# Kernel optimization log

Measured on AMD Instinct MI355X. Metric: run time of the kernel, lower is better.

Reference implementation:

```python
import jax, jax.numpy as jnp
import numpy as np

B, T, V, E, H, C = 128, 256, 50000, 300, 512, 11
START, STOP = 9, 10
NEG = -100000.0


def _lstm_dir(x, mask, w_ih, w_hh, b_ih, b_hh, reverse):
    # x: [B,T,D]; precompute input-to-gate projection for all timesteps
    gx = jnp.einsum('btd,gd->btg', x, w_ih) + b_ih + b_hh
    m = mask
    if reverse:
        gx = gx[:, ::-1]
        m = m[:, ::-1]
    Bc = x.shape[0]
    Hh = w_hh.shape[1]

    def step(carry, inp):
        h, c = carry
        g, mt = inp
        gates = g + h @ w_hh.T  # [B,4H]
        i, f, gg, o = jnp.split(gates, 4, axis=-1)
        i = jax.nn.sigmoid(i)
        f = jax.nn.sigmoid(f)
        o = jax.nn.sigmoid(o)
        gg = jnp.tanh(gg)
        c_new = f * c + i * gg
        h_new = o * jnp.tanh(c_new)
        mt = mt[:, None]
        h = jnp.where(mt, h_new, h)  # packed-sequence semantics: hold state on pads
        c = jnp.where(mt, c_new, c)
        return (h, c), h

    init = (jnp.zeros((Bc, Hh), x.dtype), jnp.zeros((Bc, Hh), x.dtype))
    _, hs = jax.lax.scan(step, init, (gx.transpose(1, 0, 2), m.T))
    hs = hs.transpose(1, 0, 2)
    if reverse:
        hs = hs[:, ::-1]
    # pad_packed_sequence zeroes padded positions
    return hs * mask[..., None].astype(x.dtype)


def _encode(tokens, mask, embeddings, params):
    x = embeddings[tokens]
    for (wif, whf, bif, bhf, wir, whr, bir, bhr) in params:
        fwd = _lstm_dir(x, mask, wif, whf, bif, bhf, False)
        bwd = _lstm_dir(x, mask, wir, whr, bir, bhr, True)
        x = jnp.concatenate([fwd, bwd], -1)
    return x


def _viterbi(emis, mask, transitions, seq_len):
    def vstep(scores, inp):
        emi, mt = inp
        cand = scores[:, :, None] + transitions[None]  # [B,C,C]
        bt = jnp.argmax(cand, axis=1)
        new = jnp.max(cand, axis=1) + emi
        return jnp.where(mt[:, None], new, scores), bt

    scores0 = jnp.zeros_like(emis[:, 0, :])
    final, backtrack = jax.lax.scan(vstep, scores0, (emis.transpose(1, 0, 2), mask.T))
    final = final + transitions[:, STOP][None]
    best_last = jnp.argmax(final, axis=-1)  # [B]

    ls = jnp.arange(emis.shape[1] - 1, -1, -1)

    def btstep(cur, inp):
        bt_l, l = inp
        emit = jnp.where(l < seq_len, cur, 0)  # pad tail with 0 as in original
        prev = jnp.take_along_axis(bt_l, cur[:, None], axis=1)[:, 0]
        cur = jnp.where((l >= 1) & (l <= seq_len - 1), prev, cur)
        return cur, emit

    _, emits = jax.lax.scan(btstep, best_last, (backtrack[::-1], ls))
    return emits[::-1].T  # [B,T]


def _nll(emis, tags, mask, transitions, seq_len):
    # CRF forward algorithm (replicates original init with -1e5 full scores)
    def fstep(scores, inp):
        emi, mt = inp
        new = jax.nn.logsumexp(scores[:, :, None] + emi[:, None, :] + transitions[None], axis=1)
        return jnp.where(mt[:, None], new, scores), None

    scores0 = jnp.full_like(emis[:, 0, :], NEG)
    final, _ = jax.lax.scan(fstep, scores0, (emis.transpose(1, 0, 2), mask.T))
    fwd_score = jax.nn.logsumexp(final + transitions[:, STOP][None], axis=-1, keepdims=True)

    em_sc = jnp.take_along_axis(emis, tags[..., None], -1)[..., 0]  # [B,T]
    y_aug = jnp.concatenate([jnp.full((tags.shape[0], 1), START, tags.dtype), tags], 1)
    tr_sc = transitions[y_aug[:, :-1], y_aug[:, 1:]]  # [B,T]
    last_tag = jnp.take_along_axis(y_aug, seq_len[:, None], 1)
    last_tr = transitions[last_tag[:, 0], STOP][:, None]
    mf = mask.astype(emis.dtype)
    gold = (mf * (em_sc + tr_sc)).sum(-1, keepdims=True) + last_tr
    return (fwd_score - gold).mean()


def setup_inputs() -> dict:
    key = jax.random.key(0)
    ks = iter(jax.random.split(key, 40))
    sl = jax.random.randint(next(ks), (B,), 1, T + 1)
    sl = -jnp.sort(-sl.at[0].set(T))  # descending, max == T (pack_padded requirement)
    mask = jnp.arange(T)[None, :] < sl[:, None]
    tokens = jax.random.randint(next(ks), (B, T), 0, V)
    tags = jax.random.randint(next(ks), (B, T), 0, 9)
    s = 1.0 / float(np.sqrt(H))

    def u(shape):
        return jax.random.uniform(next(ks), shape, jnp.float32, -s, s)

    inp = dict(tokens=tokens, seq_len=sl, mask=mask, tags=tags,
               embeddings=jax.random.normal(next(ks), (V, E), jnp.float32) * 0.1)
    G = 4 * H
    for li, d in enumerate([E, 2 * H]):
        for suf in ['', 'r']:
            inp[f'w_ih_l{li}{suf}'] = u((G, d))
            inp[f'w_hh_l{li}{suf}'] = u((G, H))
            inp[f'b_ih_l{li}{suf}'] = u((G,))
            inp[f'b_hh_l{li}{suf}'] = u((G,))
    inp['fc_w'] = u((C, 2 * H))
    inp['fc_b'] = u((C,))
    tr = jax.random.normal(next(ks), (C, C), jnp.float32)
    inp['transitions'] = tr.at[START, :].set(-1.0).at[:, STOP].set(-1.0)
    return inp


def reference(tokens, seq_len, mask, tags, embeddings,
              w_ih_l0, w_hh_l0, b_ih_l0, b_hh_l0,
              w_ih_l0r, w_hh_l0r, b_ih_l0r, b_hh_l0r,
              w_ih_l1, w_hh_l1, b_ih_l1, b_hh_l1,
              w_ih_l1r, w_hh_l1r, b_ih_l1r, b_hh_l1r,
              fc_w, fc_b, transitions):
    params = [(w_ih_l0, w_hh_l0, b_ih_l0, b_hh_l0, w_ih_l0r, w_hh_l0r, b_ih_l0r, b_hh_l0r),
              (w_ih_l1, w_hh_l1, b_ih_l1, b_hh_l1, w_ih_l1r, w_hh_l1r, b_ih_l1r, b_hh_l1r)]
    out = _encode(tokens, mask, embeddings, params)  # [B,T,2H]
    emis = jnp.einsum('bth,ch->btc', out, fc_w) + fc_b  # CRF fc (dropout=eval no-op)
    pred = _viterbi(emis, mask, transitions, seq_len)
    loss = _nll(emis, tags, mask, transitions, seq_len)
    return pred, loss
```

## Files before the change

kernel.cpp:

```cpp
#include <hip/hip_runtime.h>
#include <hip/hip_bf16.h>
#include <hip/hip_fp16.h>

#define BB   128
#define TT   256
#define EE   300
#define KP0  320
#define HH   512
#define GG   2048
#define NC   11
#define MM   (BB*TT)
#define START_TAG 9
#define STOP_TAG  10
#define NEGV (-100000.0f)

typedef _Float16 h2_t __attribute__((ext_vector_type(2)));
typedef _Float16 h4_t __attribute__((ext_vector_type(4)));
typedef _Float16 h8_t __attribute__((ext_vector_type(8)));
typedef float    f4_t __attribute__((ext_vector_type(4)));

__device__ __forceinline__ float sigf(float x) { return 1.0f / (1.0f + __expf(-x)); }

__global__ __launch_bounds__(256) void init_kernel(float* out, int* flags) {
    int t = threadIdx.x;
    if (t == 0) out[MM] = 0.0f;
    for (int i = t; i < 1024; i += 256) flags[i] = 0;
}

__global__ __launch_bounds__(256) void conv_pad_kernel(const float* __restrict__ W,
                                                       _Float16* __restrict__ O,
                                                       int K, int Kp4, int total4) {
    int idx = blockIdx.x * 256 + threadIdx.x;
    if (idx >= total4) return;
    int r = idx / Kp4, c4 = idx % Kp4, c = c4 * 4;
    h4_t v;
    if (c < K) {
        float4 f = *(const float4*)(W + (size_t)r * K + c);
        v[0] = (_Float16)f.x; v[1] = (_Float16)f.y; v[2] = (_Float16)f.z; v[3] = (_Float16)f.w;
    } else {
        v[0] = v[1] = v[2] = v[3] = (_Float16)0.0f;
    }
    *(h4_t*)(O + (size_t)r * (Kp4 * 4) + c) = v;
}

__global__ __launch_bounds__(256) void embed16_kernel(const int* __restrict__ tok,
                                                      const float* __restrict__ emb,
                                                      _Float16* __restrict__ x0,
                                                      int total4) {
    int idx = blockIdx.x * 256 + threadIdx.x;
    if (idx >= total4) return;
    int m = idx / (KP0 / 4), c4 = idx % (KP0 / 4), c = c4 * 4;
    h4_t v;
    if (c < EE) {
        float4 f = *(const float4*)(emb + (size_t)tok[m] * EE + c);
        v[0] = (_Float16)f.x; v[1] = (_Float16)f.y; v[2] = (_Float16)f.z; v[3] = (_Float16)f.w;
    } else {
        v[0] = v[1] = v[2] = v[3] = (_Float16)0.0f;
    }
    *(h4_t*)(x0 + (size_t)m * KP0 + c) = v;
}

#define LDA 72
__global__ __launch_bounds__(256) void gemm_bt_kernel(const _Float16* __restrict__ A,
                                                      const _Float16* __restrict__ Wf,
                                                      const float* __restrict__ b1,
                                                      const float* __restrict__ b2,
                                                      _Float16* __restrict__ C,
                                                      int Kp) {
    __shared__ __align__(16) char smem[36864];
    _Float16* As = (_Float16*)smem;
    _Float16* Bs = (_Float16*)(smem + 18432);
    const int tid = threadIdx.x;
    const int m0 = blockIdx.y * 128, n0 = blockIdx.x * 128;
    const int wv = tid >> 6, lane = tid & 63;
    const int wm = wv & 1, wn = wv >> 1;
    const int col = lane & 15, quad = lane >> 4;

    f4_t acc[4][4];
#pragma unroll
    for (int i = 0; i < 4; ++i)
#pragma unroll
        for (int j = 0; j < 4; ++j) acc[i][j] = (f4_t){0.f, 0.f, 0.f, 0.f};

    for (int k0 = 0; k0 < Kp; k0 += 64) {
#pragma unroll
        for (int cch = 0; cch < 4; ++cch) {
            int id = cch * 256 + tid;
            int row = id >> 3, cc = id & 7;
            h8_t va = *(const h8_t*)(A + (size_t)(m0 + row) * Kp + k0 + cc * 8);
            h8_t vb = *(const h8_t*)(Wf + (size_t)(n0 + row) * Kp + k0 + cc * 8);
            *(h8_t*)(As + row * LDA + cc * 8) = va;
            *(h8_t*)(Bs + row * LDA + cc * 8) = vb;
        }
        __syncthreads();
#pragma unroll
        for (int kk = 0; kk < 2; ++kk) {
            h8_t af[4], bf[4];
#pragma unroll
            for (int i = 0; i < 4; ++i) {
                af[i] = *(const h8_t*)(As + (wm * 64 + i * 16 + col) * LDA + kk * 32 + quad * 8);
                bf[i] = *(const h8_t*)(Bs + (wn * 64 + i * 16 + col) * LDA + kk * 32 + quad * 8);
            }
#pragma unroll
            for (int mi = 0; mi < 4; ++mi)
#pragma unroll
                for (int ni = 0; ni < 4; ++ni)
                    acc[mi][ni] = __builtin_amdgcn_mfma_f32_16x16x32_f16(af[mi], bf[ni], acc[mi][ni], 0, 0, 0);
        }
        __syncthreads();
    }

    _Float16* Ct = (_Float16*)smem;
#pragma unroll
    for (int ni = 0; ni < 4; ++ni) {
        int n = n0 + wn * 64 + ni * 16 + col;
        float bias = b1[n] + b2[n];
#pragma unroll
        for (int mi = 0; mi < 4; ++mi) {
#pragma unroll
            for (int r = 0; r < 4; ++r) {
                int mrow = wm * 64 + mi * 16 + quad * 4 + r;
                Ct[mrow * 136 + wn * 64 + ni * 16 + col] = (_Float16)(acc[mi][ni][r] + bias);
            }
        }
    }
    __syncthreads();
    {
        int row = tid >> 1, half = tid & 1;
#pragma unroll
        for (int cc2 = 0; cc2 < 8; ++cc2) {
            h8_t v = *(const h8_t*)(Ct + row * 136 + half * 64 + cc2 * 8);
            *(h8_t*)(C + (size_t)(m0 + row) * GG + n0 + half * 64 + cc2 * 8) = v;
        }
    }
}

__global__ __launch_bounds__(256, 1) void lstm_rec3_kernel(
        const _Float16* __restrict__ gx_f, const _Float16* __restrict__ gx_r,
        const float* __restrict__ whh_f, const float* __restrict__ whh_r,
        const int* __restrict__ seqlen, int c0, int nbg,
        _Float16* __restrict__ hs, _Float16* __restrict__ hbuf, int* __restrict__ flags) {
    extern __shared__ _Float16 Wlds[];
    _Float16* hstage = Wlds + 32768;

    const int wg = blockIdx.x;
    const int gs = wg & 15;
    const int grp = wg >> 4;
    const int bg = grp % nbg;
    const int dir = grp / nbg;
    const _Float16* gx = dir ? gx_r : gx_f;
    const float* W = dir ? whh_r : whh_f;
    int* myFlags = flags + grp * 16;
    _Float16* hb = hbuf + (size_t)grp * 2 * 16384;

    const int tid = threadIdx.x;
    const int wv = tid >> 6, lane = tid & 63;
    const int mt = wv & 1;
    const int p  = wv >> 1;
    const int col = lane & 15, quad = lane >> 4;

    for (int e = tid; e < 4096; e += 256) {
        int ln = e & 63, kc = (e >> 6) & 15, nt = e >> 10;
        int pp = nt >> 1;
        int n_in_pair = ((nt & 1) << 4) + (ln & 15);
        int gt = n_in_pair >> 3, jj = n_in_pair & 7;
        int R = gt * 512 + gs * 16 + pp * 8 + jj;
        int k = kc * 32 + (ln >> 4) * 8;
        const float4* src = (const float4*)(W + (size_t)R * 512 + k);
        float4 f0 = src[0], f1 = src[1];
        h8_t v;
        v[0] = (_Float16)f0.x; v[1] = (_Float16)f0.y; v[2] = (_Float16)f0.z; v[3] = (_Float16)f0.w;
        v[4] = (_Float16)f1.x; v[5] = (_Float16)f1.y; v[6] = (_Float16)f1.z; v[7] = (_Float16)f1.w;
        *(h8_t*)(Wlds + (size_t)e * 8) = v;
    }
    __syncthreads();

    const int maxsl = seqlen[c0 + bg * 32];
    int sl_r[4];
#pragma unroll
    for (int r = 0; r < 4; ++r) sl_r[r] = seqlen[c0 + bg * 32 + mt * 16 + quad * 4 + r];

    const int jglob = gs * 16 + p * 8 + (col & 7);
    const int hi = col >> 3;

    _Float16 pg0[4], pg1[4];
#pragma unroll
    for (int r = 0; r < 4; ++r) {
        pg0[r] = (_Float16)0.0f; pg1[r] = (_Float16)0.0f;
        if (0 < sl_r[r]) {
            int tm = dir ? (sl_r[r] - 1) : 0;
            int b_loc = bg * 32 + mt * 16 + quad * 4 + r;
            size_t base = ((size_t)(b_loc * TT + tm)) * GG;
            pg0[r] = gx[base + hi * 512 + jglob];
            pg1[r] = gx[base + 1024 + hi * 512 + jglob];
        }
    }

    if (tid < 128) {
        int m = tid >> 2, q = tid & 3;
        unsigned long long z = 0ull;
        const _Float16* dst = hb + 16384 + m * 512 + gs * 16 + q * 4;
        asm volatile("global_store_dwordx2 %0, %1, off sc0 sc1" :: "v"(dst), "v"(z) : "memory");
    }
    asm volatile("s_waitcnt vmcnt(0)" ::: "memory");
    __syncthreads();
    if (tid == 0) {
        int one = 1;
        asm volatile("global_store_dword %0, %1, off sc0 sc1" :: "v"(myFlags + gs), "v"(one) : "memory");
    }

    float cst[4] = {0.f, 0.f, 0.f, 0.f};
    float hst[4] = {0.f, 0.f, 0.f, 0.f};

    for (int s = 0; s < maxsl; ++s) {
        if (tid < 16) {
            const int* fp = myFlags + tid;
            int v, it = 0;
            for (;;) {
                asm volatile("global_load_dword %0, %1, off sc0 sc1\n\ts_waitcnt vmcnt(0)"
                             : "=v"(v) : "v"(fp) : "memory");
                if (v >= s + 1) break;
                if (it < 3) __builtin_amdgcn_s_sleep(1);
                else        __builtin_amdgcn_s_sleep(4);
                ++it;
            }
        }
        __syncthreads();

        const _Float16* hrd = hb + ((s + 1) & 1) * 16384;
        _Float16* hwr = hb + (s & 1) * 16384;

        h8_t a[16];
        const _Float16* ap = hrd + (mt * 16 + col) * 512 + quad * 8;
#pragma unroll
        for (int kc = 0; kc < 16; ++kc)
            asm volatile("global_load_dwordx4 %0, %1, off sc0 sc1"
                         : "=v"(a[kc]) : "v"(ap + kc * 32));
        asm volatile("s_waitcnt vmcnt(0)" ::: "memory");

        f4_t acc0 = {0.f, 0.f, 0.f, 0.f};
        f4_t acc1 = {0.f, 0.f, 0.f, 0.f};
#pragma unroll
        for (int kc = 0; kc < 16; ++kc) {
            h8_t b0 = *(const h8_t*)(Wlds + (((p * 2 + 0) * 16 + kc) * 64 + lane) * 8);
            h8_t b1 = *(const h8_t*)(Wlds + (((p * 2 + 1) * 16 + kc) * 64 + lane) * 8);
            acc0 = __builtin_amdgcn_mfma_f32_16x16x32_f16(a[kc], b0, acc0, 0, 0, 0);
            acc1 = __builtin_amdgcn_mfma_f32_16x16x32_f16(a[kc], b1, acc1, 0, 0, 0);
        }

#pragma unroll
        for (int r = 0; r < 4; ++r) {
            const bool valid = (s < sl_r[r]);
            float a0 = acc0[r] + (float)pg0[r];
            float a1 = acc1[r] + (float)pg1[r];
            float x0v = __shfl_xor(a0, 8);
            float x1v = __shfl_xor(a1, 8);
            float gi = hi ? x0v : a0;
            float gf = hi ? a0 : x0v;
            float gg2 = hi ? x1v : a1;
            float go = hi ? a1 : x1v;
            if (valid) {
                float cn = sigf(gf) * cst[r] + sigf(gi) * tanhf(gg2);
                cst[r] = cn;
                hst[r] = sigf(go) * tanhf(cn);
            }
            if (!hi)
                hstage[(mt * 16 + quad * 4 + r) * 16 + p * 8 + (col & 7)] = (_Float16)hst[r];
        }
        __syncthreads();

        if (tid < 128) {
            int m = tid >> 2, q = tid & 3;
            unsigned long long v = *(const unsigned long long*)(hstage + m * 16 + q * 4);
            const _Float16* dst = hwr + m * 512 + gs * 16 + q * 4;
            asm volatile("global_store_dwordx2 %0, %1, off sc0 sc1" :: "v"(dst), "v"(v) : "memory");
        }
        asm volatile("s_waitcnt vmcnt(0)" ::: "memory");
        __syncthreads();
        if (tid == 0) {
            int fv = s + 2;
            asm volatile("global_store_dword %0, %1, off sc0 sc1" :: "v"(myFlags + gs), "v"(fv) : "memory");
        }

#pragma unroll
        for (int r = 0; r < 4; ++r) {
            const bool valid = (s < sl_r[r]);
            if (valid && !hi) {
                int b_loc = bg * 32 + mt * 16 + quad * 4 + r;
                int tm = dir ? (sl_r[r] - 1 - s) : s;
                hs[((size_t)(b_loc * TT + tm) << 10) + (dir << 9) + jglob] = (_Float16)hst[r];
            }
        }
        {
            int sn = s + 1;
#pragma unroll
            for (int r = 0; r < 4; ++r) {
                pg0[r] = (_Float16)0.0f; pg1[r] = (_Float16)0.0f;
                if (sn < sl_r[r]) {
                    int tm = dir ? (sl_r[r] - 1 - sn) : sn;
                    int b_loc = bg * 32 + mt * 16 + quad * 4 + r;
                    size_t base = ((size_t)(b_loc * TT + tm)) * GG;
                    pg0[r] = gx[base + hi * 512 + jglob];
                    pg1[r] = gx[base + 1024 + hi * 512 + jglob];
                }
            }
        }
    }
}

__global__ __launch_bounds__(256) void emis_kernel(const _Float16* __restrict__ hs,
                                                   const float* __restrict__ fc_w,
                                                   const float* __restrict__ fc_b,
                                                   float* __restrict__ emis, int n) {
    int idx = blockIdx.x * 256 + threadIdx.x;
    if (idx >= n) return;
    int m = idx / NC, cc = idx % NC;
    const h8_t* a = (const h8_t*)(hs + (size_t)m * 1024);
    const float4* w = (const float4*)(fc_w + (size_t)cc * 1024);
    float s = 0.f;
#pragma unroll 4
    for (int k = 0; k < 128; ++k) {
        h8_t x = a[k];
        float4 y0 = w[2 * k], y1 = w[2 * k + 1];
        s += (float)x[0] * y0.x + (float)x[1] * y0.y + (float)x[2] * y0.z + (float)x[3] * y0.w;
        s += (float)x[4] * y1.x + (float)x[5] * y1.y + (float)x[6] * y1.z + (float)x[7] * y1.w;
    }
    emis[idx] = s + fc_b[cc];
}

__global__ __launch_bounds__(64) void crf_kernel(const float* __restrict__ emis,
                                                 const int* __restrict__ seq_len,
                                                 const int* __restrict__ tags,
                                                 const float* __restrict__ trans,
                                                 unsigned char* __restrict__ bt,
                                                 float* __restrict__ out, int c0) {
    const int b_loc = blockIdx.x;
    const int b = c0 + b_loc;
    const int lane = threadIdx.x;
    __shared__ float tr[NC * NC];
    for (int i = lane; i < NC * NC; i += 64) tr[i] = trans[i];
    __syncthreads();
    const int sl = seq_len[b];
    const bool act = lane < NC;
    const int jj = act ? lane : 0;

    float vs = 0.0f;
    float ns = NEGV;

    for (int t = 0; t < sl; ++t) {
        float ej = act ? emis[(size_t)(b_loc * TT + t) * NC + lane] : 0.0f;
        float vmax = -1e30f, nmax = -1e30f;
        int varg = 0;
        float nsave[NC];
#pragma unroll
        for (int i = 0; i < NC; ++i) {
            float vi = __shfl(vs, i);
            float ni = __shfl(ns, i);
            float tij = tr[i * NC + jj];
            float cv = vi + tij;
            if (cv > vmax) { vmax = cv; varg = i; }
            float cn = ni + tij;
            nsave[i] = cn;
            if (cn > nmax) nmax = cn;
        }
        float ssum = 0.f;
#pragma unroll
        for (int i = 0; i < NC; ++i) ssum += expf(nsave[i] - nmax);
        if (act) {
            vs = vmax + ej;
            ns = nmax + logf(ssum) + ej;
            bt[(size_t)(b_loc * TT + t) * NC + lane] = (unsigned char)varg;
        }
    }

    float finv = act ? vs + tr[lane * NC + STOP_TAG] : -1e30f;
    float finn = act ? ns + tr[lane * NC + STOP_TAG] : -1e30f;
    float vbest = -1e30f, fmax = -1e30f;
    int barg = 0;
#pragma unroll
    for (int j = 0; j < NC; ++j) {
        float v = __shfl(finv, j);
        if (v > vbest) { vbest = v; barg = j; }
        float n = __shfl(finn, j);
        if (n > fmax) fmax = n;
    }
    float fsum = 0.f;
#pragma unroll
    for (int j = 0; j < NC; ++j) fsum += expf(__shfl(finn, j) - fmax);
    float fwd = fmax + logf(fsum);

    float gsum = 0.f;
    for (int t = lane; t < sl; t += 64) {
        int tg = tags[b * TT + t];
        int pv = (t == 0) ? START_TAG : tags[b * TT + t - 1];
        gsum += emis[(size_t)(b_loc * TT + t) * NC + tg] + tr[pv * NC + tg];
    }
#pragma unroll
    for (int off = 32; off > 0; off >>= 1) gsum += __shfl_down(gsum, off);

    if (lane == 0) {
        float gold = gsum + tr[tags[b * TT + sl - 1] * NC + STOP_TAG];
        atomicAdd(out + MM, (fwd - gold) * (1.0f / (float)BB));
        int cur = barg;
        for (int l = sl - 1; l >= 0; --l) {
            out[b * TT + l] = (float)cur;
            if (l >= 1) cur = (int)bt[(size_t)(b_loc * TT + l) * NC + cur];
        }
    }
    for (int l = sl + lane; l < TT; l += 64) out[b * TT + l] = 0.0f;
}

extern "C" void kernel_launch(void* const* d_in, const int* in_sizes, int n_in,
                              void* d_out, int out_size, void* d_ws, size_t ws_size,
                              hipStream_t stream) {
    (void)in_sizes; (void)n_in; (void)out_size;
    const int* tokens = (const int*)d_in[0];
    const int* seqlen = (const int*)d_in[1];
    const int* tags = (const int*)d_in[3];
    const float* emb = (const float*)d_in[4];
    const float* w_ih_l0  = (const float*)d_in[5];
    const float* w_hh_l0  = (const float*)d_in[6];
    const float* b_ih_l0  = (const float*)d_in[7];
    const float* b_hh_l0  = (const float*)d_in[8];
    const float* w_ih_l0r = (const float*)d_in[9];
    const float* w_hh_l0r = (const float*)d_in[10];
    const float* b_ih_l0r = (const float*)d_in[11];
    const float* b_hh_l0r = (const float*)d_in[12];
    const float* w_ih_l1  = (const float*)d_in[13];
    const float* w_hh_l1  = (const float*)d_in[14];
    const float* b_ih_l1  = (const float*)d_in[15];
    const float* b_hh_l1  = (const float*)d_in[16];
    const float* w_ih_l1r = (const float*)d_in[17];
    const float* w_hh_l1r = (const float*)d_in[18];
    const float* b_ih_l1r = (const float*)d_in[19];
    const float* b_hh_l1r = (const float*)d_in[20];
    const float* fc_w  = (const float*)d_in[21];
    const float* fc_b  = (const float*)d_in[22];
    const float* trans = (const float*)d_in[23];

    const size_t per_b = 2097152u + 524288u + 163840u + 11264u + 2816u;
    const size_t fixed = 524288u + 4096u + 2u * 1310720u + 2u * 4194304u;
    int Bc = 128;
    while (Bc > 32 && fixed + per_b * (size_t)Bc > ws_size) Bc >>= 1;

    char* ws = (char*)d_ws;
    _Float16* hbuf = (_Float16*)ws;
    int* flags = (int*)(ws + 524288u);
    _Float16* w0f = (_Float16*)(ws + 528384u);
    _Float16* w0r = (_Float16*)(ws + 528384u + 1310720u);
    _Float16* w1f = (_Float16*)(ws + 528384u + 2u * 1310720u);
    _Float16* w1r = (_Float16*)(ws + 528384u + 2u * 1310720u + 4194304u);
    char* p = ws + fixed;
    _Float16* gxf   = (_Float16*)p;   p += (size_t)Bc * 1048576u;
    _Float16* gxr   = (_Float16*)p;   p += (size_t)Bc * 1048576u;
    _Float16* hs    = (_Float16*)p;   p += (size_t)Bc * 524288u;
    _Float16* x0f16 = (_Float16*)p;   p += (size_t)Bc * 163840u;
    float* emis     = (float*)p;      p += (size_t)Bc * 11264u;
    unsigned char* bt = (unsigned char*)p;
    float* out = (float*)d_out;

    init_kernel<<<1, 256, 0, stream>>>(out, flags);
    conv_pad_kernel<<<(2048 * 80 + 255) / 256, 256, 0, stream>>>(w_ih_l0,  w0f, EE, 80, 2048 * 80);
    conv_pad_kernel<<<(2048 * 80 + 255) / 256, 256, 0, stream>>>(w_ih_l0r, w0r, EE, 80, 2048 * 80);
    conv_pad_kernel<<<(2048 * 256 + 255) / 256, 256, 0, stream>>>(w_ih_l1,  w1f, 1024, 256, 2048 * 256);
    conv_pad_kernel<<<(2048 * 256 + 255) / 256, 256, 0, stream>>>(w_ih_l1r, w1r, 1024, 256, 2048 * 256);

    const int nbg = Bc / 32;
    const int nchunk = BB / Bc;
    for (int cidx = 0; cidx < nchunk; ++cidx) {
        const int c0 = cidx * Bc;
        const int Mc = Bc * TT;
        dim3 gdim(GG / 128, Mc / 128);
        int* fl_l0 = flags + (cidx * 2 + 0) * 128;
        int* fl_l1 = flags + (cidx * 2 + 1) * 128;

        embed16_kernel<<<(Mc * 80 + 255) / 256, 256, 0, stream>>>(tokens + c0 * TT, emb, x0f16, Mc * 80);
        gemm_bt_kernel<<<gdim, 256, 0, stream>>>(x0f16, w0f, b_ih_l0,  b_hh_l0,  gxf, KP0);
        gemm_bt_kernel<<<gdim, 256, 0, stream>>>(x0f16, w0r, b_ih_l0r, b_hh_l0r, gxr, KP0);
        lstm_rec3_kernel<<<2 * nbg * 16, 256, 66560, stream>>>(
            gxf, gxr, w_hh_l0, w_hh_l0r, seqlen, c0, nbg, hs, hbuf, fl_l0);
        gemm_bt_kernel<<<gdim, 256, 0, stream>>>(hs, w1f, b_ih_l1,  b_hh_l1,  gxf, 1024);
        gemm_bt_kernel<<<gdim, 256, 0, stream>>>(hs, w1r, b_ih_l1r, b_hh_l1r, gxr, 1024);
        lstm_rec3_kernel<<<2 * nbg * 16, 256, 66560, stream>>>(
            gxf, gxr, w_hh_l1, w_hh_l1r, seqlen, c0, nbg, hs, hbuf, fl_l1);
        emis_kernel<<<(Mc * NC + 255) / 256, 256, 0, stream>>>(hs, fc_w, fc_b, emis, Mc * NC);
        crf_kernel<<<Bc, 64, 0, stream>>>(emis, seqlen, tags, trans, bt, out, c0);
    }
}
```

Measured before the change: 5.761 ms.

## Pin LSTM recurrence groups to single XCDs with dynamic claiming and wider slices

The recurrent LSTM kernel now has each workgroup atomically claim a slot from a per-XCD counter read via the XCC_ID register. Each group's 16 workgroups therefore all sit on one XCD and can exchange hidden state through the shared L2 without system-coherent sc1 traffic. Each workgroup now covers 32 hidden units instead of 16, doubling the LDS weight footprint to 130KB, and tanh is replaced by an exp-based approximation. Unclaimed surplus blocks exit immediately. The grid is fixed at 256 blocks, and correctness assumes every XCD gets at least 16 co-resident blocks and that the cross-XCD coherence model holds.

New measurement: 9.892 ms. 1.72x slower.

```diff
diff --git a/kernel.cpp b/kernel.cpp
--- a/kernel.cpp
+++ b/kernel.cpp
@@ -20,11 +20,16 @@
 typedef float    f4_t __attribute__((ext_vector_type(4)));
 
 __device__ __forceinline__ float sigf(float x) { return 1.0f / (1.0f + __expf(-x)); }
+__device__ __forceinline__ float tanhf_fast(float x) {
+    x = fminf(fmaxf(x, -15.f), 15.f);
+    float e = __expf(2.0f * x);
+    return (e - 1.0f) / (e + 1.0f);
+}
 
 __global__ __launch_bounds__(256) void init_kernel(float* out, int* flags) {
     int t = threadIdx.x;
     if (t == 0) out[MM] = 0.0f;
-    for (int i = t; i < 1024; i += 256) flags[i] = 0;
+    for (int i = t; i < 2048; i += 256) flags[i] = 0;
 }
 
 __global__ __launch_bounds__(256) void conv_pad_kernel(const float* __restrict__ W,
@@ -135,36 +140,51 @@
     }
 }
 
-__global__ __launch_bounds__(256, 1) void lstm_rec3_kernel(
+__global__ __launch_bounds__(256, 1) void lstm_rec4_kernel(
         const _Float16* __restrict__ gx_f, const _Float16* __restrict__ gx_r,
         const float* __restrict__ whh_f, const float* __restrict__ whh_r,
         const int* __restrict__ seqlen, int c0, int nbg,
-        _Float16* __restrict__ hs, _Float16* __restrict__ hbuf, int* __restrict__ flags) {
+        _Float16* __restrict__ hs, _Float16* __restrict__ hbuf, int* __restrict__ region) {
     extern __shared__ _Float16 Wlds[];
-    _Float16* hstage = Wlds + 32768;
-
-    const int wg = blockIdx.x;
-    const int gs = wg & 15;
-    const int grp = wg >> 4;
+    _Float16* hstage = Wlds + 65536;
+    __shared__ int claim_s;
+
+    const int tid = threadIdx.x;
+    if (tid == 0) {
+        int xcd;
+        asm volatile("s_getreg_b32 %0, hwreg(HW_REG_XCC_ID)" : "=s"(xcd));
+        xcd &= 7;
+        int slot = __hip_atomic_fetch_add(region + 128 + xcd, 1,
+                                          __ATOMIC_RELAXED, __HIP_MEMORY_SCOPE_SYSTEM);
+        claim_s = (xcd << 8) | (slot < 255 ? slot : 255);
+    }
+    __syncthreads();
+    const int grp = claim_s >> 8;
+    const int gs  = claim_s & 255;
+    const int ngrp = 2 * nbg;
+    if (grp >= ngrp || gs >= 16) return;
+
     const int bg = grp % nbg;
     const int dir = grp / nbg;
     const _Float16* gx = dir ? gx_r : gx_f;
     const float* W = dir ? whh_r : whh_f;
-    int* myFlags = flags + grp * 16;
+    int* myFlags = region + grp * 16;
     _Float16* hb = hbuf + (size_t)grp * 2 * 16384;
 
-    const int tid = threadIdx.x;
     const int wv = tid >> 6, lane = tid & 63;
     const int mt = wv & 1;
     const int p  = wv >> 1;
     const int col = lane & 15, quad = lane >> 4;
 
-    for (int e = tid; e < 4096; e += 256) {
-        int ln = e & 63, kc = (e >> 6) & 15, nt = e >> 10;
-        int pp = nt >> 1;
-        int n_in_pair = ((nt & 1) << 4) + (ln & 15);
-        int gt = n_in_pair >> 3, jj = n_in_pair & 7;
-        int R = gt * 512 + gs * 16 + pp * 8 + jj;
+    for (int e = tid; e < 8192; e += 256) {
+        int ln = e & 63;
+        int kc = (e >> 6) & 15;
+        int sub = (e >> 10) & 1;
+        int pr  = (e >> 11) & 1;
+        int pp  = (e >> 12) & 1;
+        int n = ln & 15;
+        int g = pr * 2 + (n >> 3);
+        int R = g * 512 + gs * 32 + pp * 16 + sub * 8 + (n & 7);
         int k = kc * 32 + (ln >> 4) * 8;
         const float4* src = (const float4*)(W + (size_t)R * 512 + k);
         float4 f0 = src[0], f1 = src[1];
@@ -180,27 +200,31 @@
 #pragma unroll
     for (int r = 0; r < 4; ++r) sl_r[r] = seqlen[c0 + bg * 32 + mt * 16 + quad * 4 + r];
 
-    const int jglob = gs * 16 + p * 8 + (col & 7);
     const int hi = col >> 3;
-
-    _Float16 pg0[4], pg1[4];
-#pragma unroll
-    for (int r = 0; r < 4; ++r) {
-        pg0[r] = (_Float16)0.0f; pg1[r] = (_Float16)0.0f;
-        if (0 < sl_r[r]) {
-            int tm = dir ? (sl_r[r] - 1) : 0;
-            int b_loc = bg * 32 + mt * 16 + quad * 4 + r;
-            size_t base = ((size_t)(b_loc * TT + tm)) * GG;
-            pg0[r] = gx[base + hi * 512 + jglob];
-            pg1[r] = gx[base + 1024 + hi * 512 + jglob];
-        }
-    }
-
-    if (tid < 128) {
-        int m = tid >> 2, q = tid & 3;
+    int jsub[2];
+#pragma unroll
+    for (int sub = 0; sub < 2; ++sub) jsub[sub] = gs * 32 + p * 16 + sub * 8 + (col & 7);
+
+    _Float16 pg0[4][2], pg1[4][2];
+#pragma unroll
+    for (int r = 0; r < 4; ++r)
+#pragma unroll
+        for (int sub = 0; sub < 2; ++sub) {
+            pg0[r][sub] = (_Float16)0.0f; pg1[r][sub] = (_Float16)0.0f;
+            if (0 < sl_r[r]) {
+                int tm = dir ? (sl_r[r] - 1) : 0;
+                int b_loc = bg * 32 + mt * 16 + quad * 4 + r;
+                size_t base = ((size_t)(b_loc * TT + tm)) * GG;
+                pg0[r][sub] = gx[base + hi * 512 + jsub[sub]];
+                pg1[r][sub] = gx[base + 1024 + hi * 512 + jsub[sub]];
+            }
+        }
+
+    if (tid < 256) {
+        int m = tid >> 3, q = tid & 7;
         unsigned long long z = 0ull;
-        const _Float16* dst = hb + 16384 + m * 512 + gs * 16 + q * 4;
-        asm volatile("global_store_dwordx2 %0, %1, off sc0 sc1" :: "v"(dst), "v"(z) : "memory");
+        const _Float16* dst = hb + 16384 + m * 512 + gs * 32 + q * 4;
+        asm volatile("global_store_dwordx2 %0, %1, off sc0" :: "v"(dst), "v"(z) : "memory");
     }
     asm volatile("s_waitcnt vmcnt(0)" ::: "memory");
     __syncthreads();
@@ -209,8 +233,8 @@
         asm volatile("global_store_dword %0, %1, off sc0 sc1" :: "v"(myFlags + gs), "v"(one) : "memory");
     }
 
-    float cst[4] = {0.f, 0.f, 0.f, 0.f};
-    float hst[4] = {0.f, 0.f, 0.f, 0.f};
+    float cst[4][2] = {{0.f,0.f},{0.f,0.f},{0.f,0.f},{0.f,0.f}};
+    float hst[4][2] = {{0.f,0.f},{0.f,0.f},{0.f,0.f},{0.f,0.f}};
 
     for (int s = 0; s < maxsl; ++s) {
         if (tid < 16) {
@@ -234,46 +258,57 @@
         const _Float16* ap = hrd + (mt * 16 + col) * 512 + quad * 8;
 #pragma unroll
         for (int kc = 0; kc < 16; ++kc)
-            asm volatile("global_load_dwordx4 %0, %1, off sc0 sc1"
+            asm volatile("global_load_dwordx4 %0, %1, off sc0"
                          : "=v"(a[kc]) : "v"(ap + kc * 32));
         asm volatile("s_waitcnt vmcnt(0)" ::: "memory");
 
-        f4_t acc0 = {0.f, 0.f, 0.f, 0.f};
-        f4_t acc1 = {0.f, 0.f, 0.f, 0.f};
+        f4_t acc[2][2];
+#pragma unroll
+        for (int pr = 0; pr < 2; ++pr)
+#pragma unroll
+            for (int sub = 0; sub < 2; ++sub) acc[pr][sub] = (f4_t){0.f,0.f,0.f,0.f};
 #pragma unroll
         for (int kc = 0; kc < 16; ++kc) {
-            h8_t b0 = *(const h8_t*)(Wlds + (((p * 2 + 0) * 16 + kc) * 64 + lane) * 8);
-            h8_t b1 = *(const h8_t*)(Wlds + (((p * 2 + 1) * 16 + kc) * 64 + lane) * 8);
-            acc0 = __builtin_amdgcn_mfma_f32_16x16x32_f16(a[kc], b0, acc0, 0, 0, 0);
-            acc1 = __builtin_amdgcn_mfma_f32_16x16x32_f16(a[kc], b1, acc1, 0, 0, 0);
+#pragma unroll
+            for (int pr = 0; pr < 2; ++pr)
+#pragma unroll
+                for (int sub = 0; sub < 2; ++sub) {
+                    h8_t b = *(const h8_t*)(Wlds +
+                        ((size_t)(p * 4096 + pr * 2048 + sub * 1024 + kc * 64 + lane)) * 8);
+                    acc[pr][sub] = __builtin_amdgcn_mfma_f32_16x16x32_f16(a[kc], b, acc[pr][sub], 0, 0, 0);
+                }
         }
 
 #pragma unroll
         for (int r = 0; r < 4; ++r) {
             const bool valid = (s < sl_r[r]);
-            float a0 = acc0[r] + (float)pg0[r];
-            float a1 = acc1[r] + (float)pg1[r];
-            float x0v = __shfl_xor(a0, 8);
-            float x1v = __shfl_xor(a1, 8);
-            float gi = hi ? x0v : a0;
-            float gf = hi ? a0 : x0v;
-            float gg2 = hi ? x1v : a1;
-            float go = hi ? a1 : x1v;
-            if (valid) {
-                float cn = sigf(gf) * cst[r] + sigf(gi) * tanhf(gg2);
-                cst[r] = cn;
-                hst[r] = sigf(go) * tanhf(cn);
+#pragma unroll
+            for (int sub = 0; sub < 2; ++sub) {
+                float a0 = acc[0][sub][r] + (float)pg0[r][sub];
+                float a1 = acc[1][sub][r] + (float)pg1[r][sub];
+                float x0v = __shfl_xor(a0, 8);
+                float x1v = __shfl_xor(a1, 8);
+                float gi = hi ? x0v : a0;
+                float gf = hi ? a0 : x0v;
+                float gg2 = hi ? x1v : a1;
+                float go = hi ? a1 : x1v;
+                if (valid) {
+                    float cn = sigf(gf) * cst[r][sub] + sigf(gi) * tanhf_fast(gg2);
+                    cst[r][sub] = cn;
+                    hst[r][sub] = sigf(go) * tanhf_fast(cn);
+                }
+                if (!hi)
+                    hstage[(mt * 16 + quad * 4 + r) * 32 + p * 16 + sub * 8 + (col & 7)] =
+                        (_Float16)hst[r][sub];
             }
-            if (!hi)
-                hstage[(mt * 16 + quad * 4 + r) * 16 + p * 8 + (col & 7)] = (_Float16)hst[r];
         }
         __syncthreads();
 
-        if (tid < 128) {
-            int m = tid >> 2, q = tid & 3;
-            unsigned long long v = *(const unsigned long long*)(hstage + m * 16 + q * 4);
-            const _Float16* dst = hwr + m * 512 + gs * 16 + q * 4;
-            asm volatile("global_store_dwordx2 %0, %1, off sc0 sc1" :: "v"(dst), "v"(v) : "memory");
+        if (tid < 256) {
+            int m = tid >> 3, q = tid & 7;
+            unsigned long long v = *(const unsigned long long*)(hstage + m * 32 + q * 4);
+            const _Float16* dst = hwr + m * 512 + gs * 32 + q * 4;
+            asm volatile("global_store_dwordx2 %0, %1, off sc0" :: "v"(dst), "v"(v) : "memory");
         }
         asm volatile("s_waitcnt vmcnt(0)" ::: "memory");
         __syncthreads();
@@ -288,22 +323,27 @@
             if (valid && !hi) {
                 int b_loc = bg * 32 + mt * 16 + quad * 4 + r;
                 int tm = dir ? (sl_r[r] - 1 - s) : s;
-                hs[((size_t)(b_loc * TT + tm) << 10) + (dir << 9) + jglob] = (_Float16)hst[r];
+                size_t ob = ((size_t)(b_loc * TT + tm) << 10) + (dir << 9);
+#pragma unroll
+                for (int sub = 0; sub < 2; ++sub)
+                    hs[ob + jsub[sub]] = (_Float16)hst[r][sub];
             }
         }
         {
             int sn = s + 1;
 #pragma unroll
-            for (int r = 0; r < 4; ++r) {
-                pg0[r] = (_Float16)0.0f; pg1[r] = (_Float16)0.0f;
-                if (sn < sl_r[r]) {
-                    int tm = dir ? (sl_r[r] - 1 - sn) : sn;
-                    int b_loc = bg * 32 + mt * 16 + quad * 4 + r;
-                    size_t base = ((size_t)(b_loc * TT + tm)) * GG;
-                    pg0[r] = gx[base + hi * 512 + jglob];
-                    pg1[r] = gx[base + 1024 + hi * 512 + jglob];
+            for (int r = 0; r < 4; ++r)
+#pragma unroll
+                for (int sub = 0; sub < 2; ++sub) {
+                    pg0[r][sub] = (_Float16)0.0f; pg1[r][sub] = (_Float16)0.0f;
+                    if (sn < sl_r[r]) {
+                        int tm = dir ? (sl_r[r] - 1 - sn) : sn;
+                        int b_loc = bg * 32 + mt * 16 + quad * 4 + r;
+                        size_t base = ((size_t)(b_loc * TT + tm)) * GG;
+                        pg0[r][sub] = gx[base + hi * 512 + jsub[sub]];
+                        pg1[r][sub] = gx[base + 1024 + hi * 512 + jsub[sub]];
+                    }
                 }
-            }
         }
     }
 }
@@ -438,18 +478,25 @@
     const float* fc_b  = (const float*)d_in[22];
     const float* trans = (const float*)d_in[23];
 
+    static bool attr_set = false;
+    if (!attr_set) {
+        hipFuncSetAttribute((const void*)lstm_rec4_kernel,
+                            hipFuncAttributeMaxDynamicSharedMemorySize, 133120);
+        attr_set = true;
+    }
+
     const size_t per_b = 2097152u + 524288u + 163840u + 11264u + 2816u;
-    const size_t fixed = 524288u + 4096u + 2u * 1310720u + 2u * 4194304u;
+    const size_t fixed = 524288u + 8192u + 2u * 1310720u + 2u * 4194304u;
     int Bc = 128;
     while (Bc > 32 && fixed + per_b * (size_t)Bc > ws_size) Bc >>= 1;
 
     char* ws = (char*)d_ws;
     _Float16* hbuf = (_Float16*)ws;
     int* flags = (int*)(ws + 524288u);
-    _Float16* w0f = (_Float16*)(ws + 528384u);
-    _Float16* w0r = (_Float16*)(ws + 528384u + 1310720u);
-    _Float16* w1f = (_Float16*)(ws + 528384u + 2u * 1310720u);
-    _Float16* w1r = (_Float16*)(ws + 528384u + 2u * 1310720u + 4194304u);
+    _Float16* w0f = (_Float16*)(ws + 532480u);
+    _Float16* w0r = (_Float16*)(ws + 532480u + 1310720u);
+    _Float16* w1f = (_Float16*)(ws + 532480u + 2u * 1310720u);
+    _Float16* w1r = (_Float16*)(ws + 532480u + 2u * 1310720u + 4194304u);
     char* p = ws + fixed;
     _Float16* gxf   = (_Float16*)p;   p += (size_t)Bc * 1048576u;
     _Float16* gxr   = (_Float16*)p;   p += (size_t)Bc * 1048576u;
@@ -471,18 +518,18 @@
         const int c0 = cidx * Bc;
         const int Mc = Bc * TT;
         dim3 gdim(GG / 128, Mc / 128);
-        int* fl_l0 = flags + (cidx * 2 + 0) * 128;
-        int* fl_l1 = flags + (cidx * 2 + 1) * 128;
+        int* rg_l0 = flags + (cidx * 2 + 0) * 192;
+        int* rg_l1 = flags + (cidx * 2 + 1) * 192;
 
         embed16_kernel<<<(Mc * 80 + 255) / 256, 256, 0, stream>>>(tokens + c0 * TT, emb, x0f16, Mc * 80);
         gemm_bt_kernel<<<gdim, 256, 0, stream>>>(x0f16, w0f, b_ih_l0,  b_hh_l0,  gxf, KP0);
         gemm_bt_kernel<<<gdim, 256, 0, stream>>>(x0f16, w0r, b_ih_l0r, b_hh_l0r, gxr, KP0);
-        lstm_rec3_kernel<<<2 * nbg * 16, 256, 66560, stream>>>(
-            gxf, gxr, w_hh_l0, w_hh_l0r, seqlen, c0, nbg, hs, hbuf, fl_l0);
+        lstm_rec4_kernel<<<256, 256, 133120, stream>>>(
+            gxf, gxr, w_hh_l0, w_hh_l0r, seqlen, c0, nbg, hs, hbuf, rg_l0);
         gemm_bt_kernel<<<gdim, 256, 0, stream>>>(hs, w1f, b_ih_l1,  b_hh_l1,  gxf, 1024);
         gemm_bt_kernel<<<gdim, 256, 0, stream>>>(hs, w1r, b_ih_l1r, b_hh_l1r, gxr, 1024);
-        lstm_rec3_kernel<<<2 * nbg * 16, 256, 66560, stream>>>(
-            gxf, gxr, w_hh_l1, w_hh_l1r, seqlen, c0, nbg, hs, hbuf, fl_l1);
+        lstm_rec4_kernel<<<256, 256, 133120, stream>>>(
+            gxf, gxr, w_hh_l1, w_hh_l1r, seqlen, c0, nbg, hs, hbuf, rg_l1);
         emis_kernel<<<(Mc * NC + 255) / 256, 256, 0, stream>>>(hs, fc_w, fc_b, emis, Mc * NC);
         crf_kernel<<<Bc, 64, 0, stream>>>(emis, seqlen, tags, trans, bt, out, c0);
     }
```
